# Kernel optimization log

Measured on AMD Instinct MI355X. Metric: run time of the kernel, lower is better.

The kernel has to match this reference:

```python
import jax, jax.numpy as jnp
import numpy as np

CLASSES, SIZE, INPUT_SIZE, CONTEXT_SIZE, BATCH = 8, 512, 512, 512, 64
CMS = 4          # context_map_size -> 2**CMS = 16 contexts per neuron
LR = 0.01
PRED_CLIP = 0.01
WEIGHT_CLIP = 5.0


def _logit(x):
    return jnp.log(x) - jnp.log1p(-x)


def setup_inputs() -> dict:
    key = jax.random.key(0)
    k1, k2, k3, k4, k5 = jax.random.split(key, 5)
    logits = jax.random.normal(k1, (CLASSES, INPUT_SIZE, BATCH), jnp.float32)
    context = jax.random.normal(k2, (BATCH, CONTEXT_SIZE), jnp.float32)
    target = jax.random.uniform(k3, (CLASSES, BATCH), jnp.float32)
    cmaps = jax.random.normal(k4, (CLASSES, SIZE, CMS, CONTEXT_SIZE), jnp.float32)
    cmaps = cmaps / jnp.linalg.norm(cmaps, axis=-1, keepdims=True)
    cbias = jax.random.normal(k5, (CLASSES, SIZE, CMS, 1), jnp.float32)
    weights = jnp.full((CLASSES, SIZE, 2 ** CMS, INPUT_SIZE), 1.0 / INPUT_SIZE, jnp.float32)
    return {"logits": logits, "context": context, "target": target,
            "context_maps": cmaps, "context_bias": cbias, "weights": weights}


def reference(logits, context, target, context_maps, context_bias, weights):
    # --- context hashing ---
    # distances: [classes, size, cms, batch]
    distances = jnp.einsum('cskd,bd->cskb', context_maps, context)
    bits = (distances > context_bias).astype(jnp.int32)
    conv = (2 ** jnp.arange(CMS, dtype=jnp.int32))[:, None]          # [cms, 1]
    idx = jnp.sum(bits * conv, axis=-2)                              # [classes, size, batch]
    # --- gather per-context weights ---
    c = jnp.arange(CLASSES)[:, None, None]
    s = jnp.arange(SIZE)[None, :, None]
    sel = weights[c, s, idx, :]                                      # [classes, size, batch, input]
    # --- per-sample dot product (== diagonal of the original batch x batch matmul) ---
    lo = _logit(jnp.float32(PRED_CLIP))
    hi = _logit(jnp.float32(1.0 - PRED_CLIP))
    out = jnp.clip(jnp.einsum('csbi,cib->csb', sel, logits), lo, hi)  # [classes, size, batch]
    # --- online weight update (clamped) scattered back ---
    sig = jax.nn.sigmoid(out)
    diff = sig - target[:, None, :]                                  # [classes, size, batch]
    # lr * diff[c,s,b] * logits[c,i,b]  -> update [c,s,b,i]
    upd = LR * diff[:, :, :, None] * jnp.transpose(logits, (0, 2, 1))[:, None, :, :]
    new_sel = jnp.clip(sel - upd, -WEIGHT_CLIP, WEIGHT_CLIP)
    new_weights = weights.at[c, s, idx, :].set(new_sel)
    return out, new_weights
```

## Files before the change

kernel.cpp:

```cpp
#include <hip/hip_runtime.h>
#include <math.h>

#define CLASSES 8
#define SIZE 512
#define ISZ 512
#define CSZ 512
#define BATCH 64
#define CMS 4
#define NBUCKET 16
#define LR 0.01f
#define WCLIP 5.0f
#define WSTRIDE 516

__global__ __launch_bounds__(256) void pack_pre(
    const float* __restrict__ logits,
    const float* __restrict__ context,
    float* __restrict__ Lt,
    float* __restrict__ Lpk,
    float* __restrict__ ctxT4)
{
    __shared__ float t[64][65];
    const int bid  = blockIdx.x;
    const int lane = threadIdx.x & 63;
    const int w    = threadIdx.x >> 6;
    if (bid < 64) {
        const int r0 = bid << 6;
        #pragma unroll
        for (int rep = 0; rep < 16; ++rep) {
            int rr = w * 16 + rep;
            t[rr][lane] = logits[(size_t)(r0 + rr) * 64 + lane];
        }
        __syncthreads();
        const int ci = r0 + lane;
        #pragma unroll
        for (int rep = 0; rep < 16; ++rep) {
            int b = w * 16 + rep;
            float v = t[lane][b];
            Lt[(size_t)b * 4096 + ci] = v;
            Lpk[(size_t)(ci >> 2) * 256 + 4 * b + (ci & 3)] = v;
        }
    } else {
        const int c0 = (bid - 64) << 6;
        #pragma unroll
        for (int rep = 0; rep < 16; ++rep) {
            int rr = w * 16 + rep;
            t[rr][lane] = context[(size_t)rr * 512 + c0 + lane];
        }
        __syncthreads();
        #pragma unroll
        for (int rep = 0; rep < 16; ++rep) {
            int dd = c0 + w * 16 + rep;
            ctxT4[(size_t)(dd >> 2) * 256 + 4 * lane + (dd & 3)] = t[lane][w * 16 + rep];
        }
    }
}

__global__ __launch_bounds__(256, 8) void dist_kernel(
    const float* __restrict__ cmaps,
    const float* __restrict__ cbias,
    const float* __restrict__ ctxT4,
    unsigned char* __restrict__ idxOut)
{
    __shared__ int bits[CMS * BATCH];

    const int tid  = threadIdx.x;
    const int cs   = blockIdx.x;
    const int lane = tid & 63;
    const int wv   = tid >> 6;
    const int k    = __builtin_amdgcn_readfirstlane(wv);

    const float4* cmg = (const float4*)(cmaps + ((size_t)cs * CMS + k) * CSZ);
    {
        const float4* ct4 = (const float4*)ctxT4 + lane;
        float acc = 0.f;
        #pragma unroll 4
        for (int d4 = 0; d4 < 128; ++d4) {
            float4 cm4 = cmg[d4];
            float4 cv  = ct4[(size_t)d4 * 64];
            acc += cm4.x * cv.x + cm4.y * cv.y + cm4.z * cv.z + cm4.w * cv.w;
        }
        float bias = cbias[(size_t)cs * CMS + k];
        bits[k * BATCH + lane] = (acc > bias) ? 1 : 0;
    }
    __syncthreads();

    if (wv == 0) {
        int idx_b = bits[lane] | (bits[BATCH + lane] << 1) |
                    (bits[2 * BATCH + lane] << 2) | (bits[3 * BATCH + lane] << 3);
        idxOut[(size_t)cs * BATCH + lane] = (unsigned char)idx_b;
    }
}

__global__ __launch_bounds__(256, 4) void gln_bc(
    const float* __restrict__ target,
    const float* __restrict__ weights,
    const unsigned char* __restrict__ idxIn,
    const float* __restrict__ Lt,
    const float* __restrict__ Lpk,
    float* __restrict__ out,
    float* __restrict__ outW)
{
    __shared__ float Wl[NBUCKET * WSTRIDE];
    __shared__ float partial[4 * BATCH];
    __shared__ float diff_l[BATCH];
    __shared__ int   blast[NBUCKET];

    const int tid  = threadIdx.x;
    const int cs   = blockIdx.x;
    const int c    = cs >> 9;
    const int lane = tid & 63;
    const int wv   = tid >> 6;

    float4 wreg[8];
    const float4* gW = (const float4*)(weights + (size_t)cs * (NBUCKET * ISZ));
    #pragma unroll
    for (int it = 0; it < 8; ++it) wreg[it] = gW[tid + it * 256];

    const int idx_b = idxIn[(size_t)cs * BATCH + lane];

    #pragma unroll
    for (int jj = 0; jj < 4; ++jj) {
        int j = (wv << 2) + jj;
        unsigned long long m = __ballot(idx_b == j);
        if (lane == 0) blast[j] = m ? (63 - __clzll(m)) : -1;
    }

    #pragma unroll
    for (int it = 0; it < 8; ++it) {
        int f = tid + it * 256;
        *(float4*)&Wl[(f >> 7) * WSTRIDE + (f & 127) * 4] = wreg[it];
    }
    __syncthreads();

    {
        const float4* Lp4 = (const float4*)Lpk;
        const int base4 = (c * 128 + wv * 32) * 64 + lane;
        const int wb    = idx_b * WSTRIDE + wv * 128;
        float acc = 0.f;
        #pragma unroll 4
        for (int d4 = 0; d4 < 32; ++d4) {
            float4 w4 = *(const float4*)&Wl[wb + d4 * 4];
            float4 l4 = Lp4[(size_t)base4 + d4 * 64];
            acc += w4.x * l4.x + w4.y * l4.y + w4.z * l4.z + w4.w * l4.w;
        }
        partial[wv * BATCH + lane] = acc;
    }
    __syncthreads();

    if (wv == 0) {
        float s = partial[lane] + partial[BATCH + lane] +
                  partial[2 * BATCH + lane] + partial[3 * BATCH + lane];
        const float hi = 4.595119850134589f;
        float oc = fminf(fmaxf(s, -hi), hi);
        out[(size_t)cs * BATCH + lane] = oc;
        float sig = 1.f / (1.f + expf(-oc));
        diff_l[lane] = LR * (sig - target[c * BATCH + lane]);
    }
    __syncthreads();

    float* gO = outW + (size_t)cs * (NBUCKET * ISZ);
    const float* LtC = Lt + (size_t)c * ISZ;
    #pragma unroll
    for (int it = 0; it < 8; ++it) {
        int f    = tid + it * 256;
        int row  = f >> 7;
        int col4 = f & 127;
        float4 w4 = wreg[it];
        int bl = blast[row];
        float4 r = w4;
        if (bl >= 0) {
            float coef = diff_l[bl];
            float4 l4  = ((const float4*)(LtC + (size_t)bl * 4096))[col4];
            r.x = fminf(fmaxf(w4.x - coef * l4.x, -WCLIP), WCLIP);
            r.y = fminf(fmaxf(w4.y - coef * l4.y, -WCLIP), WCLIP);
            r.z = fminf(fmaxf(w4.z - coef * l4.z, -WCLIP), WCLIP);
            r.w = fminf(fmaxf(w4.w - coef * l4.w, -WCLIP), WCLIP);
        }
        ((float4*)gO)[f] = r;
    }
}

extern "C" void kernel_launch(void* const* d_in, const int* in_sizes, int n_in,
                              void* d_out, int out_size, void* d_ws, size_t ws_size,
                              hipStream_t stream) {
    const float* logits  = (const float*)d_in[0];
    const float* context = (const float*)d_in[1];
    const float* target  = (const float*)d_in[2];
    const float* cmaps   = (const float*)d_in[3];
    const float* cbias   = (const float*)d_in[4];
    const float* weights = (const float*)d_in[5];

    float* out  = (float*)d_out;
    float* outW = out + (size_t)CLASSES * SIZE * BATCH;

    float* Lt    = (float*)d_ws;
    float* Lpk   = Lt + 262144;
    float* ctxT4 = Lpk + 262144;
    unsigned char* idxb = (unsigned char*)(ctxT4 + 32768);

    pack_pre<<<72, 256, 0, stream>>>(logits, context, Lt, Lpk, ctxT4);
    dist_kernel<<<CLASSES * SIZE, 256, 0, stream>>>(cmaps, cbias, ctxT4, idxb);
    gln_bc<<<CLASSES * SIZE, 256, 0, stream>>>(target, weights, idxb, Lt, Lpk, out, outW);
}
```

Before: 140.8 us.

## Prefetch logits rows early, use nontemporal weight stores, remap dist lanes

In the update kernel, each wave computes the last-writer batch index for all 16 buckets in registers instead of through shared memory. It uses these to prefetch the needed logits rows into registers before the dot product, so that global load latency overlaps compute. The weight output is written with nontemporal stores to avoid polluting cache. The distance kernel remaps threads so each wave covers all 4 hash planes for 16 batch entries, which changes the access pattern for cmaps and the context. In exchange, register pressure rises because of an extra 8 float4s plus indices, which may reduce occupancy.

```diff
diff --git a/kernel.cpp b/kernel.cpp
--- a/kernel.cpp
+++ b/kernel.cpp
@@ -11,6 +11,8 @@
 #define LR 0.01f
 #define WCLIP 5.0f
 #define WSTRIDE 516
+
+typedef float nt_f4 __attribute__((ext_vector_type(4)));
 
 __global__ __launch_bounds__(256) void pack_pre(
     const float* __restrict__ logits,
@@ -67,11 +69,12 @@
     const int cs   = blockIdx.x;
     const int lane = tid & 63;
     const int wv   = tid >> 6;
-    const int k    = __builtin_amdgcn_readfirstlane(wv);
-
-    const float4* cmg = (const float4*)(cmaps + ((size_t)cs * CMS + k) * CSZ);
+
     {
-        const float4* ct4 = (const float4*)ctxT4 + lane;
+        const int k = lane & 3;
+        const int b = (wv << 4) | (lane >> 2);
+        const float4* cmg = (const float4*)(cmaps + ((size_t)cs * CMS + k) * CSZ);
+        const float4* ct4 = (const float4*)ctxT4 + b;
         float acc = 0.f;
         #pragma unroll 4
         for (int d4 = 0; d4 < 128; ++d4) {
@@ -80,7 +83,7 @@
             acc += cm4.x * cv.x + cm4.y * cv.y + cm4.z * cv.z + cm4.w * cv.w;
         }
         float bias = cbias[(size_t)cs * CMS + k];
-        bits[k * BATCH + lane] = (acc > bias) ? 1 : 0;
+        bits[k * BATCH + b] = (acc > bias) ? 1 : 0;
     }
     __syncthreads();
 
@@ -103,7 +106,6 @@
     __shared__ float Wl[NBUCKET * WSTRIDE];
     __shared__ float partial[4 * BATCH];
     __shared__ float diff_l[BATCH];
-    __shared__ int   blast[NBUCKET];
 
     const int tid  = threadIdx.x;
     const int cs   = blockIdx.x;
@@ -118,11 +120,24 @@
 
     const int idx_b = idxIn[(size_t)cs * BATCH + lane];
 
-    #pragma unroll
-    for (int jj = 0; jj < 4; ++jj) {
-        int j = (wv << 2) + jj;
+    int blast_r[16];
+    #pragma unroll
+    for (int j = 0; j < NBUCKET; ++j) {
         unsigned long long m = __ballot(idx_b == j);
-        if (lane == 0) blast[j] = m ? (63 - __clzll(m)) : -1;
+        blast_r[j] = m ? (63 - __clzll(m)) : -1;
+    }
+
+    const float* LtC = Lt + (size_t)c * ISZ;
+    const int col4 = tid & 127;
+    const int hi_half = (tid >> 7) & 1;
+    float4 lreg[8];
+    int    blv[8];
+    #pragma unroll
+    for (int it = 0; it < 8; ++it) {
+        int bl = hi_half ? blast_r[2 * it + 1] : blast_r[2 * it];
+        blv[it] = bl;
+        int blc = (bl >= 0) ? bl : 0;
+        lreg[it] = ((const float4*)(LtC + (size_t)blc * 4096))[col4];
     }
 
     #pragma unroll
@@ -159,24 +174,22 @@
     __syncthreads();
 
     float* gO = outW + (size_t)cs * (NBUCKET * ISZ);
-    const float* LtC = Lt + (size_t)c * ISZ;
     #pragma unroll
     for (int it = 0; it < 8; ++it) {
-        int f    = tid + it * 256;
-        int row  = f >> 7;
-        int col4 = f & 127;
+        int f = tid + it * 256;
         float4 w4 = wreg[it];
-        int bl = blast[row];
+        int bl = blv[it];
         float4 r = w4;
         if (bl >= 0) {
             float coef = diff_l[bl];
-            float4 l4  = ((const float4*)(LtC + (size_t)bl * 4096))[col4];
+            float4 l4  = lreg[it];
             r.x = fminf(fmaxf(w4.x - coef * l4.x, -WCLIP), WCLIP);
             r.y = fminf(fmaxf(w4.y - coef * l4.y, -WCLIP), WCLIP);
             r.z = fminf(fmaxf(w4.z - coef * l4.z, -WCLIP), WCLIP);
             r.w = fminf(fmaxf(w4.w - coef * l4.w, -WCLIP), WCLIP);
         }
-        ((float4*)gO)[f] = r;
+        nt_f4 rv; rv.x = r.x; rv.y = r.y; rv.z = r.z; rv.w = r.w;
+        __builtin_nontemporal_store(rv, (nt_f4*)gO + f);
     }
 }
 
```

New measurement: 350.8 us. +149.1%, slower.

## Map one wavefront per neuron with bucket-wise dot products and no LDS

Applied to the files above, without the earlier changes.

Rewrites the main kernel so that each wavefront handles one (class, neuron) pair instead of each 256-thread block doing so. Samples are grouped by context bucket via ballot, and each sample's dot product is reduced with cross-lane shuffles instead of staging weights in LDS and combining partials with block barriers. The packed logits copy (Lpk) is dropped, which saves a write in the pre-pass. In exchange, the bucket loop runs serially per sample with a six-step shuffle reduction each, and weights are loaded twice from global memory (once for the dot product, once for the update), relying on cache reuse.

```diff
diff --git a/kernel.cpp b/kernel.cpp
--- a/kernel.cpp
+++ b/kernel.cpp
@@ -10,13 +10,11 @@
 #define NBUCKET 16
 #define LR 0.01f
 #define WCLIP 5.0f
-#define WSTRIDE 516
 
 __global__ __launch_bounds__(256) void pack_pre(
     const float* __restrict__ logits,
     const float* __restrict__ context,
     float* __restrict__ Lt,
-    float* __restrict__ Lpk,
     float* __restrict__ ctxT4)
 {
     __shared__ float t[64][65];
@@ -35,9 +33,7 @@
         #pragma unroll
         for (int rep = 0; rep < 16; ++rep) {
             int b = w * 16 + rep;
-            float v = t[lane][b];
-            Lt[(size_t)b * 4096 + ci] = v;
-            Lpk[(size_t)(ci >> 2) * 256 + 4 * b + (ci & 3)] = v;
+            Lt[(size_t)b * 4096 + ci] = t[lane][b];
         }
     } else {
         const int c0 = (bid - 64) << 6;
@@ -91,93 +87,91 @@
     }
 }
 
-__global__ __launch_bounds__(256, 4) void gln_bc(
+__global__ __launch_bounds__(256, 8) void gln_bc2(
     const float* __restrict__ target,
     const float* __restrict__ weights,
     const unsigned char* __restrict__ idxIn,
     const float* __restrict__ Lt,
-    const float* __restrict__ Lpk,
     float* __restrict__ out,
     float* __restrict__ outW)
 {
-    __shared__ float Wl[NBUCKET * WSTRIDE];
-    __shared__ float partial[4 * BATCH];
-    __shared__ float diff_l[BATCH];
-    __shared__ int   blast[NBUCKET];
-
     const int tid  = threadIdx.x;
-    const int cs   = blockIdx.x;
-    const int c    = cs >> 9;
     const int lane = tid & 63;
     const int wv   = tid >> 6;
+    const int cs   = blockIdx.x * 4 + wv;
+    const int c    = cs >> 9;
 
-    float4 wreg[8];
     const float4* gW = (const float4*)(weights + (size_t)cs * (NBUCKET * ISZ));
-    #pragma unroll
-    for (int it = 0; it < 8; ++it) wreg[it] = gW[tid + it * 256];
-
     const int idx_b = idxIn[(size_t)cs * BATCH + lane];
 
-    #pragma unroll
-    for (int jj = 0; jj < 4; ++jj) {
-        int j = (wv << 2) + jj;
-        unsigned long long m = __ballot(idx_b == j);
-        if (lane == 0) blast[j] = m ? (63 - __clzll(m)) : -1;
+    float out_acc = 0.f;
+    unsigned long long m0, m1, m2, m3, m4, m5, m6, m7,
+                       m8, m9, m10, m11, m12, m13, m14, m15;
+
+#define DO_BUCKET(R, MR)                                                        \
+    {                                                                           \
+        MR = __ballot(idx_b == R);                                              \
+        unsigned long long m = MR;                                              \
+        if (m) {                                                                \
+            float4 w0 = gW[R * 128 + lane];                                     \
+            float4 w1 = gW[R * 128 + 64 + lane];                                \
+            while (m) {                                                         \
+                int b = __ffsll((unsigned long long)m) - 1;                     \
+                m &= m - 1;                                                     \
+                const float4* Lb = (const float4*)(Lt + (size_t)b * 4096 + c * 512); \
+                float4 l0 = Lb[lane];                                           \
+                float4 l1 = Lb[64 + lane];                                      \
+                float p = w0.x * l0.x + w0.y * l0.y + w0.z * l0.z + w0.w * l0.w \
+                        + w1.x * l1.x + w1.y * l1.y + w1.z * l1.z + w1.w * l1.w;\
+                p += __shfl_xor(p, 1);  p += __shfl_xor(p, 2);                  \
+                p += __shfl_xor(p, 4);  p += __shfl_xor(p, 8);                  \
+                p += __shfl_xor(p, 16); p += __shfl_xor(p, 32);                 \
+                if (lane == b) out_acc = p;                                     \
+            }                                                                   \
+        }                                                                       \
     }
+    DO_BUCKET(0, m0)   DO_BUCKET(1, m1)   DO_BUCKET(2, m2)   DO_BUCKET(3, m3)
+    DO_BUCKET(4, m4)   DO_BUCKET(5, m5)   DO_BUCKET(6, m6)   DO_BUCKET(7, m7)
+    DO_BUCKET(8, m8)   DO_BUCKET(9, m9)   DO_BUCKET(10, m10) DO_BUCKET(11, m11)
+    DO_BUCKET(12, m12) DO_BUCKET(13, m13) DO_BUCKET(14, m14) DO_BUCKET(15, m15)
+#undef DO_BUCKET
 
-    #pragma unroll
-    for (int it = 0; it < 8; ++it) {
-        int f = tid + it * 256;
-        *(float4*)&Wl[(f >> 7) * WSTRIDE + (f & 127) * 4] = wreg[it];
+    const float hi = 4.595119850134589f;
+    float oc = fminf(fmaxf(out_acc, -hi), hi);
+    out[(size_t)cs * BATCH + lane] = oc;
+    float sig = 1.f / (1.f + expf(-oc));
+    float diff = LR * (sig - target[c * BATCH + lane]);
+
+    float4* gO = (float4*)(outW + (size_t)cs * (NBUCKET * ISZ));
+
+#define UPD_BUCKET(R, MR)                                                       \
+    {                                                                           \
+        float4 w0 = gW[R * 128 + lane];                                         \
+        float4 w1 = gW[R * 128 + 64 + lane];                                    \
+        float4 r0 = w0, r1 = w1;                                                \
+        if (MR) {                                                               \
+            int bl = 63 - __clzll(MR);                                          \
+            float coef = __shfl(diff, bl);                                      \
+            const float4* Lb = (const float4*)(Lt + (size_t)bl * 4096 + c * 512); \
+            float4 l0 = Lb[lane];                                               \
+            float4 l1 = Lb[64 + lane];                                          \
+            r0.x = fminf(fmaxf(w0.x - coef * l0.x, -WCLIP), WCLIP);             \
+            r0.y = fminf(fmaxf(w0.y - coef * l0.y, -WCLIP), WCLIP);             \
+            r0.z = fminf(fmaxf(w0.z - coef * l0.z, -WCLIP), WCLIP);             \
+            r0.w = fminf(fmaxf(w0.w - coef * l0.w, -WCLIP), WCLIP);             \
+            r1.x = fminf(fmaxf(w1.x - coef * l1.x, -WCLIP), WCLIP);             \
+            r1.y = fminf(fmaxf(w1.y - coef * l1.y, -WCLIP), WCLIP);             \
+            r1.z = fminf(fmaxf(w1.z - coef * l1.z, -WCLIP), WCLIP);             \
+            r1.w = fminf(fmaxf(w1.w - coef * l1.w, -WCLIP), WCLIP);             \
+        }                                                                       \
+        gO[R * 128 + lane] = r0;                                                \
+        gO[R * 128 + 64 + lane] = r1;                                           \
     }
-    __syncthreads();
-
-    {
-        const float4* Lp4 = (const float4*)Lpk;
-        const int base4 = (c * 128 + wv * 32) * 64 + lane;
-        const int wb    = idx_b * WSTRIDE + wv * 128;
-        float acc = 0.f;
-        #pragma unroll 4
-        for (int d4 = 0; d4 < 32; ++d4) {
-            float4 w4 = *(const float4*)&Wl[wb + d4 * 4];
-            float4 l4 = Lp4[(size_t)base4 + d4 * 64];
-            acc += w4.x * l4.x + w4.y * l4.y + w4.z * l4.z + w4.w * l4.w;
-        }
-        partial[wv * BATCH + lane] = acc;
-    }
-    __syncthreads();
-
-    if (wv == 0) {
-        float s = partial[lane] + partial[BATCH + lane] +
-                  partial[2 * BATCH + lane] + partial[3 * BATCH + lane];
-        const float hi = 4.595119850134589f;
-        float oc = fminf(fmaxf(s, -hi), hi);
-        out[(size_t)cs * BATCH + lane] = oc;
-        float sig = 1.f / (1.f + expf(-oc));
-        diff_l[lane] = LR * (sig - target[c * BATCH + lane]);
-    }
-    __syncthreads();
-
-    float* gO = outW + (size_t)cs * (NBUCKET * ISZ);
-    const float* LtC = Lt + (size_t)c * ISZ;
-    #pragma unroll
-    for (int it = 0; it < 8; ++it) {
-        int f    = tid + it * 256;
-        int row  = f >> 7;
-        int col4 = f & 127;
-        float4 w4 = wreg[it];
-        int bl = blast[row];
-        float4 r = w4;
-        if (bl >= 0) {
-            float coef = diff_l[bl];
-            float4 l4  = ((const float4*)(LtC + (size_t)bl * 4096))[col4];
-            r.x = fminf(fmaxf(w4.x - coef * l4.x, -WCLIP), WCLIP);
-            r.y = fminf(fmaxf(w4.y - coef * l4.y, -WCLIP), WCLIP);
-            r.z = fminf(fmaxf(w4.z - coef * l4.z, -WCLIP), WCLIP);
-            r.w = fminf(fmaxf(w4.w - coef * l4.w, -WCLIP), WCLIP);
-        }
-        ((float4*)gO)[f] = r;
-    }
+    UPD_BUCKET(0, m0)   UPD_BUCKET(1, m1)   UPD_BUCKET(2, m2)   UPD_BUCKET(3, m3)
+    UPD_BUCKET(4, m4)   UPD_BUCKET(5, m5)   UPD_BUCKET(6, m6)   UPD_BUCKET(7, m7)
+    UPD_BUCKET(8, m8)   UPD_BUCKET(9, m9)   UPD_BUCKET(10, m10) UPD_BUCKET(11, m11)
+    UPD_BUCKET(12, m12) UPD_BUCKET(13, m13) UPD_BUCKET(14, m14) UPD_BUCKET(15, m15)
+#undef UPD_BUCKET
 }
 
 extern "C" void kernel_launch(void* const* d_in, const int* in_sizes, int n_in,
@@ -194,11 +188,10 @@
     float* outW = out + (size_t)CLASSES * SIZE * BATCH;
 
     float* Lt    = (float*)d_ws;
-    float* Lpk   = Lt + 262144;
-    float* ctxT4 = Lpk + 262144;
+    float* ctxT4 = Lt + 262144;
     unsigned char* idxb = (unsigned char*)(ctxT4 + 32768);
 
-    pack_pre<<<72, 256, 0, stream>>>(logits, context, Lt, Lpk, ctxT4);
+    pack_pre<<<72, 256, 0, stream>>>(logits, context, Lt, ctxT4);
     dist_kernel<<<CLASSES * SIZE, 256, 0, stream>>>(cmaps, cbias, ctxT4, idxb);
-    gln_bc<<<CLASSES * SIZE, 256, 0, stream>>>(target, weights, idxb, Lt, Lpk, out, outW);
+    gln_bc2<<<CLASSES * SIZE / 4, 256, 0, stream>>>(target, weights, idxb, Lt, out, outW);
 }
```

Result: slower. 163.8 us (+16.3%).

## Process two neurons per block with software-pipelined weight loads

Applied to the files above, without the earlier changes.

Each gln_bc block now handles two consecutive (class, neuron) rows and issues the second row's global weight loads while the first row's dot product and update run. The second row's weights go into the shared tile only after the first dot product finishes. The aim is to hide global-load latency behind compute and to spread per-block overhead over two rows. In exchange, register pressure doubles (16 float4 held per thread), which under launch_bounds(256,4) may cause spills or lower occupancy, and the grid is half as large.

```diff
diff --git a/kernel.cpp b/kernel.cpp
--- a/kernel.cpp
+++ b/kernel.cpp
@@ -103,39 +103,51 @@
     __shared__ float Wl[NBUCKET * WSTRIDE];
     __shared__ float partial[4 * BATCH];
     __shared__ float diff_l[BATCH];
-    __shared__ int   blast[NBUCKET];
+    __shared__ int   blastA[NBUCKET];
+    __shared__ int   blastB[NBUCKET];
 
     const int tid  = threadIdx.x;
-    const int cs   = blockIdx.x;
-    const int c    = cs >> 9;
+    const int csA  = blockIdx.x * 2;
+    const int csB  = csA + 1;
+    const int c    = csA >> 9;
     const int lane = tid & 63;
     const int wv   = tid >> 6;
 
-    float4 wreg[8];
-    const float4* gW = (const float4*)(weights + (size_t)cs * (NBUCKET * ISZ));
-    #pragma unroll
-    for (int it = 0; it < 8; ++it) wreg[it] = gW[tid + it * 256];
-
-    const int idx_b = idxIn[(size_t)cs * BATCH + lane];
+    float4 wregA[8];
+    const float4* gWA = (const float4*)(weights + (size_t)csA * (NBUCKET * ISZ));
+    #pragma unroll
+    for (int it = 0; it < 8; ++it) wregA[it] = gWA[tid + it * 256];
+
+    const int idxA = idxIn[(size_t)csA * BATCH + lane];
+    const int idxB = idxIn[(size_t)csB * BATCH + lane];
 
     #pragma unroll
     for (int jj = 0; jj < 4; ++jj) {
         int j = (wv << 2) + jj;
-        unsigned long long m = __ballot(idx_b == j);
-        if (lane == 0) blast[j] = m ? (63 - __clzll(m)) : -1;
+        unsigned long long mA = __ballot(idxA == j);
+        unsigned long long mB = __ballot(idxB == j);
+        if (lane == 0) {
+            blastA[j] = mA ? (63 - __clzll(mA)) : -1;
+            blastB[j] = mB ? (63 - __clzll(mB)) : -1;
+        }
     }
 
     #pragma unroll
     for (int it = 0; it < 8; ++it) {
         int f = tid + it * 256;
-        *(float4*)&Wl[(f >> 7) * WSTRIDE + (f & 127) * 4] = wreg[it];
-    }
-    __syncthreads();
+        *(float4*)&Wl[(f >> 7) * WSTRIDE + (f & 127) * 4] = wregA[it];
+    }
+    __syncthreads();
+
+    float4 wregB[8];
+    const float4* gWB = (const float4*)(weights + (size_t)csB * (NBUCKET * ISZ));
+    #pragma unroll
+    for (int it = 0; it < 8; ++it) wregB[it] = gWB[tid + it * 256];
 
     {
         const float4* Lp4 = (const float4*)Lpk;
         const int base4 = (c * 128 + wv * 32) * 64 + lane;
-        const int wb    = idx_b * WSTRIDE + wv * 128;
+        const int wb    = idxA * WSTRIDE + wv * 128;
         float acc = 0.f;
         #pragma unroll 4
         for (int d4 = 0; d4 < 32; ++d4) {
@@ -147,36 +159,92 @@
     }
     __syncthreads();
 
+    #pragma unroll
+    for (int it = 0; it < 8; ++it) {
+        int f = tid + it * 256;
+        *(float4*)&Wl[(f >> 7) * WSTRIDE + (f & 127) * 4] = wregB[it];
+    }
     if (wv == 0) {
         float s = partial[lane] + partial[BATCH + lane] +
                   partial[2 * BATCH + lane] + partial[3 * BATCH + lane];
         const float hi = 4.595119850134589f;
         float oc = fminf(fmaxf(s, -hi), hi);
-        out[(size_t)cs * BATCH + lane] = oc;
+        out[(size_t)csA * BATCH + lane] = oc;
         float sig = 1.f / (1.f + expf(-oc));
         diff_l[lane] = LR * (sig - target[c * BATCH + lane]);
     }
     __syncthreads();
 
-    float* gO = outW + (size_t)cs * (NBUCKET * ISZ);
     const float* LtC = Lt + (size_t)c * ISZ;
-    #pragma unroll
-    for (int it = 0; it < 8; ++it) {
-        int f    = tid + it * 256;
-        int row  = f >> 7;
-        int col4 = f & 127;
-        float4 w4 = wreg[it];
-        int bl = blast[row];
-        float4 r = w4;
-        if (bl >= 0) {
-            float coef = diff_l[bl];
-            float4 l4  = ((const float4*)(LtC + (size_t)bl * 4096))[col4];
-            r.x = fminf(fmaxf(w4.x - coef * l4.x, -WCLIP), WCLIP);
-            r.y = fminf(fmaxf(w4.y - coef * l4.y, -WCLIP), WCLIP);
-            r.z = fminf(fmaxf(w4.z - coef * l4.z, -WCLIP), WCLIP);
-            r.w = fminf(fmaxf(w4.w - coef * l4.w, -WCLIP), WCLIP);
-        }
-        ((float4*)gO)[f] = r;
+
+    {
+        float* gO = outW + (size_t)csA * (NBUCKET * ISZ);
+        #pragma unroll
+        for (int it = 0; it < 8; ++it) {
+            int f    = tid + it * 256;
+            int row  = f >> 7;
+            int col4 = f & 127;
+            float4 w4 = wregA[it];
+            int bl = blastA[row];
+            float4 r = w4;
+            if (bl >= 0) {
+                float coef = diff_l[bl];
+                float4 l4  = ((const float4*)(LtC + (size_t)bl * 4096))[col4];
+                r.x = fminf(fmaxf(w4.x - coef * l4.x, -WCLIP), WCLIP);
+                r.y = fminf(fmaxf(w4.y - coef * l4.y, -WCLIP), WCLIP);
+                r.z = fminf(fmaxf(w4.z - coef * l4.z, -WCLIP), WCLIP);
+                r.w = fminf(fmaxf(w4.w - coef * l4.w, -WCLIP), WCLIP);
+            }
+            ((float4*)gO)[f] = r;
+        }
+    }
+
+    {
+        const float4* Lp4 = (const float4*)Lpk;
+        const int base4 = (c * 128 + wv * 32) * 64 + lane;
+        const int wb    = idxB * WSTRIDE + wv * 128;
+        float acc = 0.f;
+        #pragma unroll 4
+        for (int d4 = 0; d4 < 32; ++d4) {
+            float4 w4 = *(const float4*)&Wl[wb + d4 * 4];
+            float4 l4 = Lp4[(size_t)base4 + d4 * 64];
+            acc += w4.x * l4.x + w4.y * l4.y + w4.z * l4.z + w4.w * l4.w;
+        }
+        partial[wv * BATCH + lane] = acc;
+    }
+    __syncthreads();
+
+    if (wv == 0) {
+        float s = partial[lane] + partial[BATCH + lane] +
+                  partial[2 * BATCH + lane] + partial[3 * BATCH + lane];
+        const float hi = 4.595119850134589f;
+        float oc = fminf(fmaxf(s, -hi), hi);
+        out[(size_t)csB * BATCH + lane] = oc;
+        float sig = 1.f / (1.f + expf(-oc));
+        diff_l[lane] = LR * (sig - target[c * BATCH + lane]);
+    }
+    __syncthreads();
+
+    {
+        float* gO = outW + (size_t)csB * (NBUCKET * ISZ);
+        #pragma unroll
+        for (int it = 0; it < 8; ++it) {
+            int f    = tid + it * 256;
+            int row  = f >> 7;
+            int col4 = f & 127;
+            float4 w4 = wregB[it];
+            int bl = blastB[row];
+            float4 r = w4;
+            if (bl >= 0) {
+                float coef = diff_l[bl];
+                float4 l4  = ((const float4*)(LtC + (size_t)bl * 4096))[col4];
+                r.x = fminf(fmaxf(w4.x - coef * l4.x, -WCLIP), WCLIP);
+                r.y = fminf(fmaxf(w4.y - coef * l4.y, -WCLIP), WCLIP);
+                r.z = fminf(fmaxf(w4.z - coef * l4.z, -WCLIP), WCLIP);
+                r.w = fminf(fmaxf(w4.w - coef * l4.w, -WCLIP), WCLIP);
+            }
+            ((float4*)gO)[f] = r;
+        }
     }
 }
 
@@ -200,5 +268,5 @@
 
     pack_pre<<<72, 256, 0, stream>>>(logits, context, Lt, Lpk, ctxT4);
     dist_kernel<<<CLASSES * SIZE, 256, 0, stream>>>(cmaps, cbias, ctxT4, idxb);
-    gln_bc<<<CLASSES * SIZE, 256, 0, stream>>>(target, weights, idxb, Lt, Lpk, out, outW);
-}
+    gln_bc<<<CLASSES * SIZE / 2, 256, 0, stream>>>(target, weights, idxb, Lt, Lpk, out, outW);
+}
```

Result: slower. 147.2 us (+4.5%).
